# Kernel tuning notes

Hardware: AMD Instinct MI355X
Metric: run time of the kernel (lower is better)

The kernel has to match this reference:

```python
import jax, jax.numpy as jnp
import numpy as np

L, BAT, A, B, D, NBITS = 2, 32, 64, 1024, 128, 1024
PADDING = 0


def setup_inputs() -> dict:
    key = jax.random.key(0)
    k1, k2, k3, k4, k5 = jax.random.split(key, 5)
    query_embed = jax.random.normal(k1, (L, BAT, A, D), dtype=jnp.float32)
    doc_embed = jax.random.normal(k2, (L, BAT, B, D), dtype=jnp.float32)
    query_tok = jax.random.randint(k3, (BAT, A), 0, 2)
    doc_tok = jax.random.randint(k4, (BAT, B), 0, 2)
    # LSH projection matrix: randn * sigma + mu with sigma=0.1, mu=0
    r = jax.random.normal(k5, (NBITS, D), dtype=jnp.float32) * 0.1
    return {"query_embed": query_embed, "doc_embed": doc_embed,
            "query_tok": query_tok, "doc_tok": doc_tok, "r": r}


def reference(query_embed, doc_embed, query_tok, doc_tok, r):
    d = r.shape[0]  # num_bits
    # sign-hash: (emb @ r.T > 0).float()  -> binary codes in {0,1}
    c1 = (jnp.einsum('lbad,kd->lbak', query_embed, r) > 0).astype(jnp.float32)  # [L,BAT,A,NBITS]
    c2 = (jnp.einsum('lbcd,kd->lbck', doc_embed, r) > 0).astype(jnp.float32)    # [L,BAT,B,NBITS]
    # Hamming distance via popcount identity: |u-v|_H = sum(u) + sum(v) - 2 u.v
    s1 = c1.sum(-1)  # [L,BAT,A]
    s2 = c2.sum(-1)  # [L,BAT,B]
    dot = jnp.einsum('lbak,lbck->lbac', c1, c2)  # [L,BAT,A,B]
    ham = s1[..., :, None] + s2[..., None, :] - 2.0 * dot
    sim = jnp.cos(jnp.pi / d * ham)  # [L,BAT,A,B]
    # zero out padded query / doc positions
    qmask = (query_tok == PADDING)[None, :, :, None]
    dmask = (doc_tok == PADDING)[None, :, None, :]
    sim = jnp.where(qmask | dmask, 0.0, sim)
    # torch.stack(simmat, dim=1) -> [BAT, L, A, B]
    return jnp.transpose(sim, (1, 0, 2, 3))
```

## Files before the change

kernel.cpp:

```cpp
#include <hip/hip_runtime.h>
#include <math.h>

#define L_ 2
#define BAT_ 32
#define A_ 64
#define B_ 1024
#define D_ 128
#define NBITS_ 1024
#define NW 32
#define NQROWS (L_*BAT_*A_)
#define NDROWS (L_*BAT_*B_)
#define NROWS (NQROWS + NDROWS)
#define NAGRP (NROWS / 16)
#define NBGRP (NBITS_ / 16)

#define TM 128
#define TN 128
#define NXB (NROWS / TM)
#define NYB (NBITS_ / TN)
#define XPX (NXB / 8)

typedef __bf16 bf16x8 __attribute__((ext_vector_type(8)));
typedef float  f32x4  __attribute__((ext_vector_type(4)));

__global__ __launch_bounds__(256) void preswz_kernel(
    const float* __restrict__ qe, const float* __restrict__ de,
    const float* __restrict__ r, __bf16* __restrict__ asw,
    __bf16* __restrict__ rsw)
{
    const int g = blockIdx.x;
    const int t = threadIdx.x;
    const int ks = t >> 7, kk = (t >> 6) & 1, quad = (t >> 4) & 3, col = t & 15;

    const float* src;
    __bf16* dst;
    if (g < NAGRP) {
        int row = g * 16 + col;
        src = (row < NQROWS) ? (qe + (size_t)row * D_)
                             : (de + (size_t)(row - NQROWS) * D_);
        dst = asw + (size_t)g * 4096;
    } else {
        int bit = (g - NAGRP) * 16 + col;
        src = r + (size_t)bit * D_;
        dst = rsw + (size_t)(g - NAGRP) * 4096;
    }

    const int ko = ks * 64 + kk * 32 + quad * 8;
    float4 v0 = *(const float4*)(src + ko);
    float4 v1 = *(const float4*)(src + ko + 4);
    bf16x8 hi, lo;
    hi[0] = (__bf16)v0.x; hi[1] = (__bf16)v0.y;
    hi[2] = (__bf16)v0.z; hi[3] = (__bf16)v0.w;
    hi[4] = (__bf16)v1.x; hi[5] = (__bf16)v1.y;
    hi[6] = (__bf16)v1.z; hi[7] = (__bf16)v1.w;
    lo[0] = (__bf16)(v0.x - (float)hi[0]);
    lo[1] = (__bf16)(v0.y - (float)hi[1]);
    lo[2] = (__bf16)(v0.z - (float)hi[2]);
    lo[3] = (__bf16)(v0.w - (float)hi[3]);
    lo[4] = (__bf16)(v1.x - (float)hi[4]);
    lo[5] = (__bf16)(v1.y - (float)hi[5]);
    lo[6] = (__bf16)(v1.z - (float)hi[6]);
    lo[7] = (__bf16)(v1.w - (float)hi[7]);

    const int c_hi = ks * 16 + kk * 4 + quad;
    const int c_lo = c_hi + 8;
    *(bf16x8*)(dst + (size_t)(c_hi * 16 + col) * 8) = hi;
    *(bf16x8*)(dst + (size_t)(c_lo * 16 + col) * 8) = lo;
}

__global__ __launch_bounds__(512, 4) void hash_kernel(
    const __bf16* __restrict__ asw, const __bf16* __restrict__ rsw,
    unsigned int* __restrict__ codes_t)
{
    const int t = threadIdx.x;
    const int lane = t & 63;
    const int quad = lane >> 4;
    const int col  = lane & 15;
    const int wv   = __builtin_amdgcn_readfirstlane(t >> 6);

    const int bid = blockIdx.x;
    const int xcd = bid & 7;
    const int s   = bid >> 3;
    const int bx  = xcd * XPX + (s >> 3);
    const int by  = s & 7;

    const int wrow = (wv >> 1) * 32;
    const int wbit = (wv & 1) * 64;
    const int ga0 = (bx * TM + wrow) >> 4;
    const int gb0 = (by * TN + wbit) >> 4;

    f32x4 acc[2][4];
    #pragma unroll
    for (int ti = 0; ti < 2; ++ti)
        #pragma unroll
        for (int tj = 0; tj < 4; ++tj)
            acc[ti][tj] = (f32x4){0.f, 0.f, 0.f, 0.f};

    #pragma unroll
    for (int ks = 0; ks < 2; ++ks) {
        #pragma unroll
        for (int kk = 0; kk < 2; ++kk) {
            const int cbi_h = ks * 4 + kk;
            const int cbi_l = cbi_h + 2;
            bf16x8 ahi[2], bhi[4], alo[2], blo[4];
            #pragma unroll
            for (int ti = 0; ti < 2; ++ti)
                ahi[ti] = *(const bf16x8*)(
                    asw + (((size_t)(ga0 + ti) * 8 + cbi_h) * 64 + lane) * 8);
            #pragma unroll
            for (int tj = 0; tj < 4; ++tj)
                bhi[tj] = *(const bf16x8*)(
                    rsw + (((size_t)(gb0 + tj) * 8 + cbi_h) * 64 + lane) * 8);
            #pragma unroll
            for (int ti = 0; ti < 2; ++ti)
                #pragma unroll
                for (int tj = 0; tj < 4; ++tj)
                    acc[ti][tj] = __builtin_amdgcn_mfma_f32_16x16x32_bf16(
                        ahi[ti], bhi[tj], acc[ti][tj], 0, 0, 0);
            #pragma unroll
            for (int ti = 0; ti < 2; ++ti)
                alo[ti] = *(const bf16x8*)(
                    asw + (((size_t)(ga0 + ti) * 8 + cbi_l) * 64 + lane) * 8);
            #pragma unroll
            for (int ti = 0; ti < 2; ++ti)
                #pragma unroll
                for (int tj = 0; tj < 4; ++tj)
                    acc[ti][tj] = __builtin_amdgcn_mfma_f32_16x16x32_bf16(
                        alo[ti], bhi[tj], acc[ti][tj], 0, 0, 0);
            #pragma unroll
            for (int tj = 0; tj < 4; ++tj)
                blo[tj] = *(const bf16x8*)(
                    rsw + (((size_t)(gb0 + tj) * 8 + cbi_l) * 64 + lane) * 8);
            #pragma unroll
            for (int ti = 0; ti < 2; ++ti)
                #pragma unroll
                for (int tj = 0; tj < 4; ++tj)
                    acc[ti][tj] = __builtin_amdgcn_mfma_f32_16x16x32_bf16(
                        ahi[ti], blo[tj], acc[ti][tj], 0, 0, 0);
        }
    }

    const int row0 = bx * TM;
    #pragma unroll
    for (int ti = 0; ti < 2; ++ti) {
        #pragma unroll
        for (int rg = 0; rg < 4; ++rg) {
            unsigned long long b[4];
            #pragma unroll
            for (int tj = 0; tj < 4; ++tj)
                b[tj] = __ballot(acc[ti][tj][rg] > 0.f);
            if (col < 2) {
                const int w = col;
                unsigned int lo16 = (unsigned int)(b[2 * w]     >> (16 * quad)) & 0xFFFFu;
                unsigned int hi16 = (unsigned int)(b[2 * w + 1] >> (16 * quad)) & 0xFFFFu;
                const int row = row0 + wrow + ti * 16 + quad * 4 + rg;
                const int wg  = by * 4 + (wv & 1) * 2 + w;
                codes_t[(size_t)wg * NROWS + row] = lo16 | (hi16 << 16);
            }
        }
    }
}

__global__ __launch_bounds__(256) void simmat_kernel(
    const unsigned int* __restrict__ codes_t,
    const int* __restrict__ qtok, const int* __restrict__ dtok,
    float* __restrict__ out)
{
    __shared__ unsigned int qc[8 * 36];

    const int blk  = blockIdx.x;
    const int ct   = blk & 3;
    const int asub = (blk >> 2) & 7;
    const int b    = (blk >> 5) & 31;
    const int l    = blk >> 10;
    const int t    = threadIdx.x;

    const int a0 = asub * 8;
    const int qrow0 = (l * BAT_ + b) * A_ + a0;
    if (t < 256) {
        int w = t >> 3, a = t & 7;
        qc[a * 36 + w] = codes_t[(size_t)w * NROWS + qrow0 + a];
    }
    __syncthreads();

    const int c = ct * 256 + t;
    const size_t drow = (size_t)NQROWS + (size_t)(l * BAT_ + b) * B_ + c;
    unsigned int dc[NW];
    #pragma unroll
    for (int w = 0; w < NW; ++w) dc[w] = codes_t[(size_t)w * NROWS + drow];
    const float dm = (dtok[b * B_ + c] != 0) ? 1.f : 0.f;

    float* obase = out + ((size_t)((b * L_ + l) * A_ + a0)) * B_ + c;
    #pragma unroll
    for (int ai = 0; ai < 8; ++ai) {
        int ham = 0;
        #pragma unroll
        for (int m = 0; m < 8; ++m) {
            uint4 qv = *(const uint4*)(&qc[ai * 36 + m * 4]);
            ham += __popc(qv.x ^ dc[4 * m])     + __popc(qv.y ^ dc[4 * m + 1])
                 + __popc(qv.z ^ dc[4 * m + 2]) + __popc(qv.w ^ dc[4 * m + 3]);
        }
        const float qmv = (qtok[b * A_ + a0 + ai] != 0) ? 1.f : 0.f;
        float sim = __cosf((float)M_PI / (float)NBITS_ * (float)ham);
        obase[(size_t)ai * B_] = sim * (qmv * dm);
    }
}

extern "C" void kernel_launch(void* const* d_in, const int* in_sizes, int n_in,
                              void* d_out, int out_size, void* d_ws, size_t ws_size,
                              hipStream_t stream) {
    const float* qe  = (const float*)d_in[0];
    const float* de  = (const float*)d_in[1];
    const int* qtok  = (const int*)d_in[2];
    const int* dtok  = (const int*)d_in[3];
    const float* r   = (const float*)d_in[4];
    float* out = (float*)d_out;

    unsigned int* codes_t = (unsigned int*)d_ws;
    __bf16* rsw = (__bf16*)((char*)d_ws + 8912896);
    __bf16* asw = (__bf16*)((char*)d_ws + 8912896 + 524288);

    preswz_kernel<<<NAGRP + NBGRP, 256, 0, stream>>>(qe, de, r, asw, rsw);
    hash_kernel<<<NXB * NYB, 512, 0, stream>>>(asw, rsw, codes_t);
    simmat_kernel<<<L_ * BAT_ * 8 * 4, 256, 0, stream>>>(codes_t, qtok, dtok, out);
}
```

Measured before the change: 166.8 us.

## Stage projection tile in LDS via direct global-to-LDS loads and prefetch A fragments

The hash GEMM kernel now copies its block's 64KB slice of the swizzled projection matrix into shared memory with global_load_lds before computing, so the B fragments are read from LDS instead of global memory by each wave. The A fragments are software-prefetched one k-chunk ahead in registers, with hi and lo pairs loaded together. This is meant to cut redundant global/L2 traffic for the shared B operand and to hide load latency behind MFMAs. In exchange it uses 64KB of LDS per block, which limits occupancy to fewer blocks per CU than the launch bound asks for, and adds a block barrier.

```diff
diff --git a/kernel.cpp b/kernel.cpp
--- a/kernel.cpp
+++ b/kernel.cpp
@@ -72,6 +72,8 @@
     const __bf16* __restrict__ asw, const __bf16* __restrict__ rsw,
     unsigned int* __restrict__ codes_t)
 {
+    __shared__ __align__(16) unsigned char bsh[65536];
+
     const int t = threadIdx.x;
     const int lane = t & 63;
     const int quad = lane >> 4;
@@ -85,9 +87,29 @@
     const int by  = s & 7;
 
     const int wrow = (wv >> 1) * 32;
-    const int wbit = (wv & 1) * 64;
+    const int half = wv & 1;
     const int ga0 = (bx * TM + wrow) >> 4;
-    const int gb0 = (by * TN + wbit) >> 4;
+
+    const __bf16* abase = asw + (size_t)ga0 * 4096 + (size_t)lane * 8;
+#define ALOAD(ti, cbi) (*(const bf16x8*)(abase + ((ti) * 8 + (cbi)) * 512))
+
+    const unsigned char* bbase = bsh + half * 32768 + lane * 16;
+#define BLOAD(tj, cbi) (*(const bf16x8*)(bbase + (tj) * 8192 + (cbi) * 1024))
+
+    bf16x8 xh0 = ALOAD(0, 0), xh1 = ALOAD(1, 0);
+    bf16x8 xl0 = ALOAD(0, 2), xl1 = ALOAD(1, 2);
+    bf16x8 yh0, yh1, yl0, yl1;
+
+    {
+        const char* bsrc = (const char*)rsw + (size_t)by * 65536 + (size_t)t * 16;
+        #pragma unroll
+        for (int i = 0; i < 8; ++i)
+            __builtin_amdgcn_global_load_lds(
+                (const __attribute__((address_space(1))) unsigned int*)(bsrc + i * 8192),
+                (__attribute__((address_space(3))) unsigned int*)(bsh + i * 8192 + t * 16),
+                16, 0, 0);
+    }
+    __syncthreads();
 
     f32x4 acc[2][4];
     #pragma unroll
@@ -96,49 +118,42 @@
         for (int tj = 0; tj < 4; ++tj)
             acc[ti][tj] = (f32x4){0.f, 0.f, 0.f, 0.f};
 
-    #pragma unroll
-    for (int ks = 0; ks < 2; ++ks) {
-        #pragma unroll
-        for (int kk = 0; kk < 2; ++kk) {
-            const int cbi_h = ks * 4 + kk;
-            const int cbi_l = cbi_h + 2;
-            bf16x8 ahi[2], bhi[4], alo[2], blo[4];
-            #pragma unroll
-            for (int ti = 0; ti < 2; ++ti)
-                ahi[ti] = *(const bf16x8*)(
-                    asw + (((size_t)(ga0 + ti) * 8 + cbi_h) * 64 + lane) * 8);
-            #pragma unroll
-            for (int tj = 0; tj < 4; ++tj)
-                bhi[tj] = *(const bf16x8*)(
-                    rsw + (((size_t)(gb0 + tj) * 8 + cbi_h) * 64 + lane) * 8);
-            #pragma unroll
-            for (int ti = 0; ti < 2; ++ti)
-                #pragma unroll
-                for (int tj = 0; tj < 4; ++tj)
-                    acc[ti][tj] = __builtin_amdgcn_mfma_f32_16x16x32_bf16(
-                        ahi[ti], bhi[tj], acc[ti][tj], 0, 0, 0);
-            #pragma unroll
-            for (int ti = 0; ti < 2; ++ti)
-                alo[ti] = *(const bf16x8*)(
-                    asw + (((size_t)(ga0 + ti) * 8 + cbi_l) * 64 + lane) * 8);
-            #pragma unroll
-            for (int ti = 0; ti < 2; ++ti)
-                #pragma unroll
-                for (int tj = 0; tj < 4; ++tj)
-                    acc[ti][tj] = __builtin_amdgcn_mfma_f32_16x16x32_bf16(
-                        alo[ti], bhi[tj], acc[ti][tj], 0, 0, 0);
-            #pragma unroll
-            for (int tj = 0; tj < 4; ++tj)
-                blo[tj] = *(const bf16x8*)(
-                    rsw + (((size_t)(gb0 + tj) * 8 + cbi_l) * 64 + lane) * 8);
-            #pragma unroll
-            for (int ti = 0; ti < 2; ++ti)
-                #pragma unroll
-                for (int tj = 0; tj < 4; ++tj)
-                    acc[ti][tj] = __builtin_amdgcn_mfma_f32_16x16x32_bf16(
-                        ahi[ti], blo[tj], acc[ti][tj], 0, 0, 0);
-        }
-    }
+#define MFMA __builtin_amdgcn_mfma_f32_16x16x32_bf16
+#define BATCH(A0, A1, B0, B1, B2, B3)                       \
+    acc[0][0] = MFMA(A0, B0, acc[0][0], 0, 0, 0);           \
+    acc[0][1] = MFMA(A0, B1, acc[0][1], 0, 0, 0);           \
+    acc[0][2] = MFMA(A0, B2, acc[0][2], 0, 0, 0);           \
+    acc[0][3] = MFMA(A0, B3, acc[0][3], 0, 0, 0);           \
+    acc[1][0] = MFMA(A1, B0, acc[1][0], 0, 0, 0);           \
+    acc[1][1] = MFMA(A1, B1, acc[1][1], 0, 0, 0);           \
+    acc[1][2] = MFMA(A1, B2, acc[1][2], 0, 0, 0);           \
+    acc[1][3] = MFMA(A1, B3, acc[1][3], 0, 0, 0);
+
+#define ITER(CH, cH0, cH1, cL0, cL1, DO_PREF, NH, nH0, nH1, nL0, nL1)   \
+    {                                                                    \
+        if (DO_PREF) {                                                   \
+            nH0 = ALOAD(0, NH);       nH1 = ALOAD(1, NH);                \
+            nL0 = ALOAD(0, (NH) + 2); nL1 = ALOAD(1, (NH) + 2);          \
+        }                                                                \
+        bf16x8 b0 = BLOAD(0, CH), b1 = BLOAD(1, CH),                     \
+               b2 = BLOAD(2, CH), b3 = BLOAD(3, CH);                     \
+        BATCH(cH0, cH1, b0, b1, b2, b3)                       \
+        BATCH(cL0, cL1, b0, b1, b2, b3)                       \
+        b0 = BLOAD(0, (CH) + 2); b1 = BLOAD(1, (CH) + 2);                \
+        b2 = BLOAD(2, (CH) + 2); b3 = BLOAD(3, (CH) + 2);                \
+        BATCH(cH0, cH1, b0, b1, b2, b3)                       \
+    }
+
+    ITER(0, xh0, xh1, xl0, xl1, 1, 1, yh0, yh1, yl0, yl1)
+    ITER(1, yh0, yh1, yl0, yl1, 1, 4, xh0, xh1, xl0, xl1)
+    ITER(4, xh0, xh1, xl0, xl1, 1, 5, yh0, yh1, yl0, yl1)
+    ITER(5, yh0, yh1, yl0, yl1, 0, 0, xh0, xh1, xl0, xl1)
+
+#undef ITER
+#undef BATCH
+#undef MFMA
+#undef BLOAD
+#undef ALOAD
 
     const int row0 = bx * TM;
     #pragma unroll
@@ -154,7 +169,7 @@
                 unsigned int lo16 = (unsigned int)(b[2 * w]     >> (16 * quad)) & 0xFFFFu;
                 unsigned int hi16 = (unsigned int)(b[2 * w + 1] >> (16 * quad)) & 0xFFFFu;
                 const int row = row0 + wrow + ti * 16 + quad * 4 + rg;
-                const int wg  = by * 4 + (wv & 1) * 2 + w;
+                const int wg  = by * 4 + half * 2 + w;
                 codes_t[(size_t)wg * NROWS + row] = lo16 | (hi16 << 16);
             }
         }
```

After: 154.7 us. 1.08x faster.
